# Optimization experiments

Hardware: AMD Instinct MI355X
Metric: run time of the kernel (lower is better)

## Reference

```python
import jax, jax.numpy as jnp
import numpy as np
import itertools

N_OBJECTS = 8
NUM_VARS = 2  # num_total_variables


def _perm_indices(num_objects: int, num_vars: int):
    """Static permutation indices, matching AndLayer.build()."""
    perm_idxs = np.array(list(itertools.permutations(range(num_objects), num_vars)))  # [K, V]
    binary_idxs = np.stack(np.nonzero(1 - np.eye(num_vars))).T  # [V*(V-1), 2]
    binary_idxs = binary_idxs.reshape(num_vars, num_vars - 1, 2)
    perm_bidxs = perm_idxs[:, binary_idxs]  # [K, V, V-1, 2]
    shift = (perm_bidxs[..., 1] > perm_bidxs[..., 0]).astype(np.int64)
    perm_bidxs = np.stack([perm_bidxs[..., 0], perm_bidxs[..., 1] - shift], axis=-1)
    return perm_idxs, perm_bidxs


def setup_inputs() -> dict:
    key = jax.random.key(0)
    k0, k1, k2, k3 = jax.random.split(key, 4)
    B, N, P0, P1, P2, C = 32, N_OBJECTS, 64, 128, 64, 128
    V = NUM_VARS
    num_in = P0 + V * P1 + V * (V - 1) * P2  # 448
    return {
        "nullary_preds": jax.random.uniform(k0, (B, P0), dtype=jnp.float32),
        "unary_preds": jax.random.uniform(k1, (B, N, P1), dtype=jnp.float32),
        "binary_preds": jax.random.uniform(k2, (B, N, N - 1, P2), dtype=jnp.float32),
        "kernel": jax.random.normal(k3, (num_in, C), dtype=jnp.float32),
    }


def reference(nullary_preds, unary_preds, binary_preds, kernel):
    B = nullary_preds.shape[0]
    N = unary_preds.shape[1]
    perm_idxs, perm_bidxs = _perm_indices(N, NUM_VARS)
    K = perm_idxs.shape[0]  # number of permutations

    # [B, K, P0]
    perm_nullary = jnp.broadcast_to(nullary_preds[:, None], (B, K) + nullary_preds.shape[1:])
    # gather over object axis: [B, K, V, P1]
    perm_unary = unary_preds[:, perm_idxs]
    # gather (i, j') pairs: [B, K, V, V-1, P2]
    perm_binary = binary_preds[:, perm_bidxs[..., 0], perm_bidxs[..., 1]]

    in_tensor = jnp.concatenate(
        [perm_nullary,
         perm_unary.reshape(B, K, -1),
         perm_binary.reshape(B, K, -1)], axis=-1)  # [B, K, num_in]

    k = jnp.tanh(kernel)  # [num_in, C]
    # [B, K, num_in, C]
    weighted_truth = in_tensor[..., None] * k + (1.0 - jnp.square(k))
    conjuncts = jnp.max(jnp.min(weighted_truth, axis=2), axis=1)  # [B, C]
    return conjuncts
```

## Files before the change

kernel.cpp:

```cpp
#include <hip/hip_runtime.h>
#include <math.h>

#define BATCH   32
#define NOBJ    8
#define P0      64
#define P1      128
#define P2      64
#define COUT    128
#define KPERM   56
#define ITOT    448
#define NBG     4
#define IC      16

#define TK_ELEMS  (ITOT * COUT)
#define X_ELEMS   (KPERM * 8 * ITOT * 4)

__device__ __forceinline__ unsigned enc_f32(float f) {
    unsigned b = __float_as_uint(f);
    return (b & 0x80000000u) ? ~b : (b | 0x80000000u);
}

__global__ __launch_bounds__(256) void prep(const float* __restrict__ nullary,
                                            const float* __restrict__ unary,
                                            const float* __restrict__ binary,
                                            const float* __restrict__ kern,
                                            float* __restrict__ tk,
                                            float* __restrict__ X,
                                            unsigned* __restrict__ amax) {
    const int blk = blockIdx.x;
    const int tid = threadIdx.x;

    if (blk < KPERM * NBG) {
        const int k  = blk >> 2;
        const int bg = blk & 3;
        const int a = k / (NOBJ - 1);
        const int r = k % (NOBJ - 1);
        const int bobj = r + (r >= a ? 1 : 0);
        const int m0 = bobj - (bobj > a ? 1 : 0);
        const int m1 = a - (a > bobj ? 1 : 0);

        for (int e = tid; e < ITOT * 8; e += 256) {
            const int i  = e >> 3;
            const int lb = e & 7;
            const int b  = bg * 8 + lb;
            float v;
            if (i < P0) {
                v = nullary[b * P0 + i];
            } else if (i < P0 + 2 * P1) {
                const int t2 = i - P0;
                const int vv = t2 >> 7;
                const int p  = t2 & (P1 - 1);
                const int n  = vv ? bobj : a;
                v = unary[(b * NOBJ + n) * P1 + p];
            } else {
                const int t2 = i - (P0 + 2 * P1);
                const int vv = t2 >> 6;
                const int p  = t2 & (P2 - 1);
                const int n  = vv ? bobj : a;
                const int m  = vv ? m1 : m0;
                v = binary[((b * NOBJ + n) * (NOBJ - 1) + m) * P2 + p];
            }
            const int g = bg * 2 + (lb >> 2);
            const int j = lb & 3;
            X[((k * 8 + g) * ITOT + i) * 4 + j] = v;
        }
    } else {
        const int tb = blk - KPERM * NBG;
        const int idx0 = tb * 256 + tid;
        #pragma unroll
        for (int it = 0; it < 7; ++it) {
            const int idx = idx0 + it * 8192;
            tk[idx] = tanhf(kern[idx]);
        }
        if (tb < 16) amax[idx0] = 0u;
    }
}

__global__ __launch_bounds__(256) void and_main(const float* __restrict__ tk,
                                                const float* __restrict__ X,
                                                unsigned* __restrict__ amax) {
    const int blk = blockIdx.x;
    const int k   = blk >> 2;
    const int bg  = blk & 3;
    const int tid = threadIdx.x;
    const int c   = tid & (COUT - 1);
    const int h   = tid >> 7;
    const int g   = bg * 2 + h;

    const int fbase = __builtin_amdgcn_readfirstlane((k * 8 + g) * ITOT);
    const float4* __restrict__ Xg = ((const float4*)X) + fbase;
    const float* __restrict__ tkp = tk + c;

    float acc0 = INFINITY, acc1 = INFINITY, acc2 = INFINITY, acc3 = INFINITY;

    for (int i0 = 0; i0 < ITOT; i0 += IC) {
        float  tv[IC];
        float4 xv[IC];
        #pragma unroll
        for (int u = 0; u < IC; ++u) tv[u] = tkp[(i0 + u) << 7];
        #pragma unroll
        for (int u = 0; u < IC; ++u) xv[u] = Xg[i0 + u];
        #pragma unroll
        for (int u = 0; u < IC; ++u) {
            const float t  = tv[u];
            const float bs = fmaf(-t, t, 1.0f);
            acc0 = fminf(acc0, fmaf(xv[u].x, t, bs));
            acc1 = fminf(acc1, fmaf(xv[u].y, t, bs));
            acc2 = fminf(acc2, fmaf(xv[u].z, t, bs));
            acc3 = fminf(acc3, fmaf(xv[u].w, t, bs));
        }
    }

    unsigned* base = amax + (g * 4) * COUT + c;
    atomicMax(base + 0 * COUT, enc_f32(acc0));
    atomicMax(base + 1 * COUT, enc_f32(acc1));
    atomicMax(base + 2 * COUT, enc_f32(acc2));
    atomicMax(base + 3 * COUT, enc_f32(acc3));
}

__global__ __launch_bounds__(256) void decode(const unsigned* __restrict__ amax,
                                              float* __restrict__ out) {
    const int idx = blockIdx.x * 256 + threadIdx.x;
    const unsigned u = amax[idx];
    const unsigned b = (u & 0x80000000u) ? (u ^ 0x80000000u) : ~u;
    out[idx] = __uint_as_float(b);
}

extern "C" void kernel_launch(void* const* d_in, const int* in_sizes, int n_in,
                              void* d_out, int out_size, void* d_ws, size_t ws_size,
                              hipStream_t stream) {
    const float* nullary = (const float*)d_in[0];
    const float* unary   = (const float*)d_in[1];
    const float* binary  = (const float*)d_in[2];
    const float* kern    = (const float*)d_in[3];
    float* out = (float*)d_out;

    float*    tk   = (float*)d_ws;
    float*    X    = tk + TK_ELEMS;
    unsigned* amax = (unsigned*)(X + X_ELEMS);

    prep<<<256, 256, 0, stream>>>(nullary, unary, binary, kern, tk, X, amax);
    and_main<<<KPERM * NBG, 256, 0, stream>>>(tk, X, amax);
    decode<<<16, 256, 0, stream>>>(amax, out);
}
```

Before: 82.64 us.

## Fuse gather into main kernel via LDS and fold decode into last block

The permuted input gather now happens inside the main kernel, which stages it in shared memory instead of writing a large X buffer to global memory in the prep kernel. The main kernel uses 512 threads that split the input dimension into four segments and reduce the partial minima through shared memory. The separate decode launch is removed: a global counter picks the last block, which decodes the atomic max results into the output. This cuts one launch and the global round trip of X, at the cost of a redundant per-block gather and an extra atomic counter with fences.

```diff
diff --git a/kernel.cpp b/kernel.cpp
--- a/kernel.cpp
+++ b/kernel.cpp
@@ -9,121 +9,131 @@
 #define COUT    128
 #define KPERM   56
 #define ITOT    448
-#define NBG     4
+#define NBG     8
+#define NIH     4
+#define ISEG    (ITOT / NIH)
 #define IC      16
 
-#define TK_ELEMS  (ITOT * COUT)
-#define X_ELEMS   (KPERM * 8 * ITOT * 4)
+#define AMAX_ELEMS 4096
+#define TK_OFF     4352
+#define TK_ELEMS   (ITOT * COUT)
 
 __device__ __forceinline__ unsigned enc_f32(float f) {
     unsigned b = __float_as_uint(f);
     return (b & 0x80000000u) ? ~b : (b | 0x80000000u);
 }
-
-__global__ __launch_bounds__(256) void prep(const float* __restrict__ nullary,
-                                            const float* __restrict__ unary,
-                                            const float* __restrict__ binary,
-                                            const float* __restrict__ kern,
-                                            float* __restrict__ tk,
-                                            float* __restrict__ X,
-                                            unsigned* __restrict__ amax) {
-    const int blk = blockIdx.x;
-    const int tid = threadIdx.x;
-
-    if (blk < KPERM * NBG) {
-        const int k  = blk >> 2;
-        const int bg = blk & 3;
-        const int a = k / (NOBJ - 1);
-        const int r = k % (NOBJ - 1);
-        const int bobj = r + (r >= a ? 1 : 0);
-        const int m0 = bobj - (bobj > a ? 1 : 0);
-        const int m1 = a - (a > bobj ? 1 : 0);
-
-        for (int e = tid; e < ITOT * 8; e += 256) {
-            const int i  = e >> 3;
-            const int lb = e & 7;
-            const int b  = bg * 8 + lb;
-            float v;
-            if (i < P0) {
-                v = nullary[b * P0 + i];
-            } else if (i < P0 + 2 * P1) {
-                const int t2 = i - P0;
-                const int vv = t2 >> 7;
-                const int p  = t2 & (P1 - 1);
-                const int n  = vv ? bobj : a;
-                v = unary[(b * NOBJ + n) * P1 + p];
-            } else {
-                const int t2 = i - (P0 + 2 * P1);
-                const int vv = t2 >> 6;
-                const int p  = t2 & (P2 - 1);
-                const int n  = vv ? bobj : a;
-                const int m  = vv ? m1 : m0;
-                v = binary[((b * NOBJ + n) * (NOBJ - 1) + m) * P2 + p];
-            }
-            const int g = bg * 2 + (lb >> 2);
-            const int j = lb & 3;
-            X[((k * 8 + g) * ITOT + i) * 4 + j] = v;
-        }
-    } else {
-        const int tb = blk - KPERM * NBG;
-        const int idx0 = tb * 256 + tid;
-        #pragma unroll
-        for (int it = 0; it < 7; ++it) {
-            const int idx = idx0 + it * 8192;
-            tk[idx] = tanhf(kern[idx]);
-        }
-        if (tb < 16) amax[idx0] = 0u;
-    }
+__device__ __forceinline__ float dec_f32(unsigned u) {
+    unsigned b = (u & 0x80000000u) ? (u ^ 0x80000000u) : ~u;
+    return __uint_as_float(b);
 }
 
-__global__ __launch_bounds__(256) void and_main(const float* __restrict__ tk,
-                                                const float* __restrict__ X,
-                                                unsigned* __restrict__ amax) {
+__global__ __launch_bounds__(256) void prep(const float* __restrict__ kern,
+                                            float* __restrict__ tk,
+                                            unsigned* __restrict__ amax) {
+    const int idx = blockIdx.x * 256 + threadIdx.x;
+    tk[idx] = tanhf(kern[idx]);
+    if (idx < AMAX_ELEMS + 1) amax[idx] = 0u;
+}
+
+__global__ __launch_bounds__(512) void and_main(const float* __restrict__ nullary,
+                                                const float* __restrict__ unary,
+                                                const float* __restrict__ binary,
+                                                const float* __restrict__ tk,
+                                                unsigned* __restrict__ amax,
+                                                unsigned* __restrict__ counter,
+                                                float* __restrict__ out) {
+    __shared__ float4 xs[ITOT];
+    __shared__ float4 pm[NIH][COUT];
+    __shared__ unsigned lastflag;
+
     const int blk = blockIdx.x;
-    const int k   = blk >> 2;
-    const int bg  = blk & 3;
+    const int k   = blk >> 3;
+    const int bg  = blk & 7;
     const int tid = threadIdx.x;
     const int c   = tid & (COUT - 1);
-    const int h   = tid >> 7;
-    const int g   = bg * 2 + h;
+    const int ih  = tid >> 7;
 
-    const int fbase = __builtin_amdgcn_readfirstlane((k * 8 + g) * ITOT);
-    const float4* __restrict__ Xg = ((const float4*)X) + fbase;
+    const int a = k / (NOBJ - 1);
+    const int r = k % (NOBJ - 1);
+    const int bobj = r + (r >= a ? 1 : 0);
+    const int m0 = bobj - (bobj > a ? 1 : 0);
+    const int m1 = a - (a > bobj ? 1 : 0);
+
+    float* xsf = (float*)xs;
+    for (int e = tid; e < ITOT * 4; e += 512) {
+        const int i = e >> 2;
+        const int j = e & 3;
+        const int b = bg * 4 + j;
+        float v;
+        if (i < P0) {
+            v = nullary[b * P0 + i];
+        } else if (i < P0 + 2 * P1) {
+            const int t2 = i - P0;
+            const int vv = t2 >> 7;
+            const int p  = t2 & (P1 - 1);
+            const int n  = vv ? bobj : a;
+            v = unary[(b * NOBJ + n) * P1 + p];
+        } else {
+            const int t2 = i - (P0 + 2 * P1);
+            const int vv = t2 >> 6;
+            const int p  = t2 & (P2 - 1);
+            const int n  = vv ? bobj : a;
+            const int m  = vv ? m1 : m0;
+            v = binary[((b * NOBJ + n) * (NOBJ - 1) + m) * P2 + p];
+        }
+        xsf[e] = v;
+    }
+    __syncthreads();
+
     const float* __restrict__ tkp = tk + c;
-
     float acc0 = INFINITY, acc1 = INFINITY, acc2 = INFINITY, acc3 = INFINITY;
 
-    for (int i0 = 0; i0 < ITOT; i0 += IC) {
-        float  tv[IC];
-        float4 xv[IC];
+    const int ibase = ih * ISEG;
+    for (int i0 = ibase; i0 < ibase + ISEG; i0 += IC) {
+        float tv[IC];
         #pragma unroll
         for (int u = 0; u < IC; ++u) tv[u] = tkp[(i0 + u) << 7];
-        #pragma unroll
-        for (int u = 0; u < IC; ++u) xv[u] = Xg[i0 + u];
         #pragma unroll
         for (int u = 0; u < IC; ++u) {
             const float t  = tv[u];
             const float bs = fmaf(-t, t, 1.0f);
-            acc0 = fminf(acc0, fmaf(xv[u].x, t, bs));
-            acc1 = fminf(acc1, fmaf(xv[u].y, t, bs));
-            acc2 = fminf(acc2, fmaf(xv[u].z, t, bs));
-            acc3 = fminf(acc3, fmaf(xv[u].w, t, bs));
+            const float4 x = xs[i0 + u];
+            acc0 = fminf(acc0, fmaf(x.x, t, bs));
+            acc1 = fminf(acc1, fmaf(x.y, t, bs));
+            acc2 = fminf(acc2, fmaf(x.z, t, bs));
+            acc3 = fminf(acc3, fmaf(x.w, t, bs));
         }
     }
 
-    unsigned* base = amax + (g * 4) * COUT + c;
-    atomicMax(base + 0 * COUT, enc_f32(acc0));
-    atomicMax(base + 1 * COUT, enc_f32(acc1));
-    atomicMax(base + 2 * COUT, enc_f32(acc2));
-    atomicMax(base + 3 * COUT, enc_f32(acc3));
-}
+    pm[ih][c] = make_float4(acc0, acc1, acc2, acc3);
+    __syncthreads();
 
-__global__ __launch_bounds__(256) void decode(const unsigned* __restrict__ amax,
-                                              float* __restrict__ out) {
-    const int idx = blockIdx.x * 256 + threadIdx.x;
-    const unsigned u = amax[idx];
-    const unsigned b = (u & 0x80000000u) ? (u ^ 0x80000000u) : ~u;
-    out[idx] = __uint_as_float(b);
+    if (ih == 0) {
+        const float4 p0 = pm[0][c], p1 = pm[1][c], p2 = pm[2][c], p3 = pm[3][c];
+        const float m0f = fminf(fminf(p0.x, p1.x), fminf(p2.x, p3.x));
+        const float m1f = fminf(fminf(p0.y, p1.y), fminf(p2.y, p3.y));
+        const float m2f = fminf(fminf(p0.z, p1.z), fminf(p2.z, p3.z));
+        const float m3f = fminf(fminf(p0.w, p1.w), fminf(p2.w, p3.w));
+        unsigned* base = amax + (bg * 4) * COUT + c;
+        atomicMax(base + 0 * COUT, enc_f32(m0f));
+        atomicMax(base + 1 * COUT, enc_f32(m1f));
+        atomicMax(base + 2 * COUT, enc_f32(m2f));
+        atomicMax(base + 3 * COUT, enc_f32(m3f));
+    }
+
+    __syncthreads();
+    if (tid == 0) {
+        __threadfence();
+        lastflag = (atomicAdd(counter, 1u) == (unsigned)(KPERM * NBG - 1));
+    }
+    __syncthreads();
+    if (lastflag) {
+        __threadfence();
+        for (int e = tid; e < AMAX_ELEMS; e += 512) {
+            const unsigned u = atomicAdd(amax + e, 0u);
+            out[e] = dec_f32(u);
+        }
+    }
 }
 
 extern "C" void kernel_launch(void* const* d_in, const int* in_sizes, int n_in,
@@ -135,11 +145,11 @@
     const float* kern    = (const float*)d_in[3];
     float* out = (float*)d_out;
 
-    float*    tk   = (float*)d_ws;
-    float*    X    = tk + TK_ELEMS;
-    unsigned* amax = (unsigned*)(X + X_ELEMS);
+    unsigned* amax    = (unsigned*)d_ws;
+    unsigned* counter = amax + AMAX_ELEMS;
+    float*    tk      = (float*)d_ws + TK_OFF;
 
-    prep<<<256, 256, 0, stream>>>(nullary, unary, binary, kern, tk, X, amax);
-    and_main<<<KPERM * NBG, 256, 0, stream>>>(tk, X, amax);
-    decode<<<16, 256, 0, stream>>>(amax, out);
+    prep<<<TK_ELEMS / 256, 256, 0, stream>>>(kern, tk, amax);
+    and_main<<<KPERM * NBG, 512, 0, stream>>>(nullary, unary, binary, tk,
+                                              amax, counter, out);
 }
```

After: 79.09 us. 1.04x faster.
